# Optimization experiments

Measured on AMD Instinct MI355X. Metric: run time of the kernel, lower is better.

The kernel has to match this reference:

```python
import jax, jax.numpy as jnp
import numpy as np

EPS = 1e-5

def _ln(x, g, b):
    mu = jnp.mean(x, axis=-1, keepdims=True)
    var = jnp.mean((x - mu) ** 2, axis=-1, keepdims=True)
    return (x - mu) / jnp.sqrt(var + EPS) * g + b

def _silu(x):
    return x * jax.nn.sigmoid(x)

def setup_inputs() -> dict:
    key = jax.random.key(0)
    ks = jax.random.split(key, 32)
    B = 131072
    def rn(k, shape, scale=0.05):
        return jax.random.normal(k, shape, dtype=jnp.float32) * scale
    inp = {
        'x': jax.random.normal(ks[0], (B, 90), dtype=jnp.float32),
        'w_emb': rn(ks[1], (24, 10)),
        'pos_d': rn(ks[2], (9, 24), 0.02),
        'pos_c': rn(ks[3], (3, 64), 0.02),
        'tw1': rn(ks[4], (256, 72)), 'tb1': rn(ks[5], (256,)),
        'tw2': rn(ks[6], (256, 256)), 'tb2': rn(ks[7], (256,)),
        'tw3': rn(ks[8], (64, 256)), 'tb3': jnp.zeros((64,), jnp.float32),
        'ln1g': jnp.ones((64,), jnp.float32), 'ln1b': jnp.zeros((64,), jnp.float32),
        'inpw': rn(ks[9], (192, 64)), 'inpb': rn(ks[10], (192,)),
        'outw': rn(ks[11], (64, 64)), 'outb': rn(ks[12], (64,)),
        'ln2g': jnp.ones((64,), jnp.float32), 'ln2b': jnp.zeros((64,), jnp.float32),
        'ffw1': rn(ks[13], (128, 64)), 'ffb1': rn(ks[14], (128,)),
        'ffw2': rn(ks[15], (64, 128)), 'ffb2': rn(ks[16], (64,)),
        'hw1': rn(ks[17], (160, 192)), 'hb1': rn(ks[18], (160,)),
        'hw2': rn(ks[19], (64, 160)), 'hb2': rn(ks[20], (64,)),
        'hw3': rn(ks[21], (1, 64)), 'hb3': jnp.zeros((1,), jnp.float32),
    }
    return inp

def reference(x, w_emb, pos_d, pos_c, tw1, tb1, tw2, tb2, tw3, tb3,
              ln1g, ln1b, inpw, inpb, outw, outb, ln2g, ln2b,
              ffw1, ffb1, ffw2, ffb2, hw1, hb1, hw2, hb2, hw3, hb3):
    B = x.shape[0]
    H, D = 4, 16  # heads, head_dim (embed 64)
    digits = x.reshape(B, 9, 10) @ w_emb.T + pos_d          # [B,9,24]
    chunks = digits.reshape(B, 3, 72)                        # [B,3,72]
    h = _silu(chunks @ tw1.T + tb1)                          # [B,3,256]
    h = _silu(h @ tw2.T + tb2)                               # [B,3,256]
    chunks = h @ tw3.T + tb3                                 # [B,3,64]
    chunks = chunks + pos_c
    a = _ln(chunks, ln1g, ln1b)
    qkv = a @ inpw.T + inpb                                  # [B,3,192]
    q, k, v = jnp.split(qkv, 3, axis=-1)
    q = q.reshape(B, 3, H, D).transpose(0, 2, 1, 3)
    k = k.reshape(B, 3, H, D).transpose(0, 2, 1, 3)
    v = v.reshape(B, 3, H, D).transpose(0, 2, 1, 3)
    scores = jnp.einsum('bhsd,bhtd->bhst', q, k) / jnp.sqrt(jnp.float32(D))
    attn = jax.nn.softmax(scores, axis=-1)
    o = jnp.einsum('bhst,bhtd->bhsd', attn, v)
    o = o.transpose(0, 2, 1, 3).reshape(B, 3, 64)
    attn_out = o @ outw.T + outb
    chunks = chunks + attn_out
    f = _ln(chunks, ln2g, ln2b)
    chunks = chunks + (_silu(f @ ffw1.T + ffb1) @ ffw2.T + ffb2)
    flat = chunks.reshape(B, 192)
    hh = _silu(flat @ hw1.T + hb1)
    hh = _silu(hh @ hw2.T + hb2)
    return hh @ hw3.T + hb3                                  # [B,1]
```

## Files before the change

kernel.cpp:

```cpp
#include <hip/hip_runtime.h>
#include <math.h>


typedef short s8v __attribute__((ext_vector_type(8)));
typedef float f4v __attribute__((ext_vector_type(4)));
typedef int   i2v __attribute__((ext_vector_type(2)));
typedef int   i4v __attribute__((ext_vector_type(4)));

__device__ __forceinline__ short f2bf(float f) {
    unsigned u = __float_as_uint(f);
    unsigned r = (u + 0x7fffu + ((u >> 16) & 1u)) >> 16;
    return (short)r;
}
__device__ __forceinline__ int cvt_pk_bf16(float a, float b) {
    int r;
    asm("v_cvt_pk_bf16_f32 %0, %1, %2" : "=v"(r) : "v"(a), "v"(b));
    return r;
}
__device__ __forceinline__ float silu_f(float v) {
    return v * __builtin_amdgcn_rcpf(1.0f + __expf(-v));
}

#define BARRIER() do {                                        \
    asm volatile("s_waitcnt lgkmcnt(0)" ::: "memory");        \
    __builtin_amdgcn_s_barrier();                             \
    __builtin_amdgcn_sched_barrier(0);                        \
} while (0)

#define OFF_T1F  0
#define OFF_TW2  8192
#define OFF_TW3  73728
#define OFF_INP  90112
#define OFF_OUT  102400
#define OFF_FF1  106496
#define OFF_FF2  114688
#define OFF_HW1  122880
#define OFF_HW2  153600
#define BIAS1_ELEM 163840

__global__ void pack_weights(const float* __restrict__ w_emb, const float* __restrict__ tw1,
                             const float* __restrict__ pos_d, const float* __restrict__ tb1,
                             const float* __restrict__ tw2, const float* __restrict__ tw3,
                             const float* __restrict__ inpw, const float* __restrict__ outw,
                             const float* __restrict__ ffw1, const float* __restrict__ ffw2,
                             const float* __restrict__ hw1, const float* __restrict__ hw2,
                             short* __restrict__ dst)
{
    int L = blockIdx.y;
    if (L == 0) {
        int total = 16 * 512;
        for (int e = blockIdx.x * blockDim.x + threadIdx.x; e < total; e += gridDim.x * blockDim.x) {
            int nt = e >> 9, q = e & 511;
            int l = q >> 3, j = q & 7;
            int n = nt * 16 + (l & 15);
            int k = (l >> 4) * 8 + j;
            float v = 0.f;
            if (k < 30) {
                int gl = k / 10, kk = k - gl * 10;
                const float* trow = tw1 + n * 72 + gl * 24;
                for (int jj = 0; jj < 24; ++jj) v += trow[jj] * w_emb[jj * 10 + kk];
            }
            dst[OFF_T1F + e] = f2bf(v);
        }
        return;
    }
    if (L == 9) {
        float* b1 = (float*)(dst + BIAS1_ELEM);
        for (int e = blockIdx.x * blockDim.x + threadIdx.x; e < 768; e += gridDim.x * blockDim.x) {
            int pos = e >> 8, n = e & 255;
            float v = tb1[n];
            for (int j = 0; j < 72; ++j)
                v += tw1[n * 72 + j] * pos_d[(pos * 3 + j / 24) * 24 + (j % 24)];
            b1[e] = v;
        }
        return;
    }
    const float* W; int K, KS, N, off;
    switch (L) {
      case 1: W = tw2;  K = 256; KS = 8; N = 256; off = OFF_TW2; break;
      case 2: W = tw3;  K = 256; KS = 8; N = 64;  off = OFF_TW3; break;
      case 3: W = inpw; K = 64;  KS = 2; N = 192; off = OFF_INP; break;
      case 4: W = outw; K = 64;  KS = 2; N = 64;  off = OFF_OUT; break;
      case 5: W = ffw1; K = 64;  KS = 2; N = 128; off = OFF_FF1; break;
      case 6: W = ffw2; K = 128; KS = 4; N = 64;  off = OFF_FF2; break;
      case 7: W = hw1;  K = 192; KS = 6; N = 160; off = OFF_HW1; break;
      default:W = hw2;  K = 160; KS = 5; N = 64;  off = OFF_HW2; break;
    }
    int total = (N >> 4) * KS * 512;
    for (int e = blockIdx.x * blockDim.x + threadIdx.x; e < total; e += gridDim.x * blockDim.x) {
        int nt = e / (KS * 512);
        int r  = e - nt * (KS * 512);
        int ks = r >> 9;
        int q  = r & 511;
        int l  = q >> 3, j = q & 7;
        int n  = nt * 16 + (l & 15);
        int k  = ks * 32 + (l >> 4) * 8 + j;
        dst[off + e] = f2bf((k < K) ? W[n * K + k] : 0.0f);
    }
}

template<int KSH> struct PreW { s8v w[KSH]; };

template<int KSH>
__device__ __forceinline__ PreW<KSH> preloadW(const short* __restrict__ Wp,
                                              int lane, int nt, int ksTotal) {
    PreW<KSH> p;
    #pragma unroll
    for (int ks = 0; ks < KSH; ++ks)
        p.w[ks] = *(const s8v*)(Wp + nt * (ksTotal * 512) + ks * 512 + lane * 8);
    return p;
}

template<int EPI, int OP>
__device__ __forceinline__ void epi_store(f4v acc, f4v bv, int t, int n0, void* Out,
                                          const float* __restrict__ aux)
{
    if (EPI == 0 || EPI == 1) {
        float v0 = acc[0] + bv[0], v1 = acc[1] + bv[1];
        float v2 = acc[2] + bv[2], v3 = acc[3] + bv[3];
        if (EPI == 0) { v0 = silu_f(v0); v1 = silu_f(v1); v2 = silu_f(v2); v3 = silu_f(v3); }
        i2v pk; pk[0] = cvt_pk_bf16(v0, v1); pk[1] = cvt_pk_bf16(v2, v3);
        *(i2v*)((short*)Out + t * OP + n0) = pk;
    } else if (EPI == 2) {
        f4v* p = (f4v*)((float*)Out + t * OP + n0);
        f4v o = *p;
        #pragma unroll
        for (int i = 0; i < 4; ++i) o[i] += acc[i] + bv[i];
        *p = o;
    } else if (EPI == 3) {
        f4v pc = *(const f4v*)(aux + (t % 3) * 64 + n0);
        f4v o;
        #pragma unroll
        for (int i = 0; i < 4; ++i) o[i] = acc[i] + bv[i] + pc[i];
        *(f4v*)((float*)Out + t * OP + n0) = o;
    } else if (EPI == 5) {
        f4v ch = *(const f4v*)(aux + t * 68 + n0);
        int rr = t / 3, cc = t - rr * 3;
        i2v pk;
        pk[0] = cvt_pk_bf16(ch[0] + acc[0] + bv[0], ch[1] + acc[1] + bv[1]);
        pk[1] = cvt_pk_bf16(ch[2] + acc[2] + bv[2], ch[3] + acc[3] + bv[3]);
        *(i2v*)((short*)Out + rr * OP + cc * 64 + n0) = pk;
    } else if (EPI == 6) {
        f4v w = *(const f4v*)(aux + n0);
        float p = silu_f(acc[0] + bv[0]) * w[0] + silu_f(acc[1] + bv[1]) * w[1]
                + silu_f(acc[2] + bv[2]) * w[2] + silu_f(acc[3] + bv[3]) * w[3];
        ((float*)Out)[t * OP + (n0 >> 2)] = p;
    } else {
        f4v bp = *(const f4v*)(aux + (t % 3) * 256 + n0);
        float v0 = silu_f(acc[0] + bp[0]), v1 = silu_f(acc[1] + bp[1]);
        float v2 = silu_f(acc[2] + bp[2]), v3 = silu_f(acc[3] + bp[3]);
        i2v pk; pk[0] = cvt_pk_bf16(v0, v1); pk[1] = cvt_pk_bf16(v2, v3);
        *(i2v*)((short*)Out + t * OP + n0) = pk;
    }
}

template<int MT, int KS, int EPI, int AP, int OP>
__device__ __forceinline__ void mfma_T(
    const short* __restrict__ Wp,
    const float* __restrict__ bias,
    const short* A, void* Out, int N,
    const float* __restrict__ aux, int lane, int wid, PreW<KS> pre)
{
    const int l15 = lane & 15, l4 = lane >> 4;
    s8v xf[MT][KS];
    #pragma unroll
    for (int m = 0; m < MT; ++m)
        #pragma unroll
        for (int ks = 0; ks < KS; ++ks)
            xf[m][ks] = *(const s8v*)(A + (m * 16 + l15) * AP + ks * 32 + l4 * 8);

    s8v wf[KS];
    #pragma unroll
    for (int ks = 0; ks < KS; ++ks) wf[ks] = pre.w[ks];

    const int NT = N >> 4;
    for (int nt = wid; nt < NT; nt += 4) {
        s8v wfn[KS];
        const bool more = (nt + 4) < NT;
        if (more) {
            #pragma unroll
            for (int ks = 0; ks < KS; ++ks)
                wfn[ks] = *(const s8v*)(Wp + (nt + 4) * (KS * 512) + ks * 512 + lane * 8);
        }
        const int n0 = nt * 16 + l4 * 4;
        f4v bv = {0.f, 0.f, 0.f, 0.f};
        if (EPI != 7) bv = *(const f4v*)(bias + n0);
        #pragma unroll
        for (int m = 0; m < MT; ++m) {
            f4v acc = {0.f, 0.f, 0.f, 0.f};
            #pragma unroll
            for (int ks = 0; ks < KS; ++ks)
                acc = __builtin_amdgcn_mfma_f32_16x16x32_bf16(wf[ks], xf[m][ks], acc, 0, 0, 0);
            epi_store<EPI, OP>(acc, bv, m * 16 + l15, n0, Out, aux);
        }
        if (more) {
            #pragma unroll
            for (int ks = 0; ks < KS; ++ks) wf[ks] = wfn[ks];
        }
    }
}

template<int OP>
__device__ __forceinline__ void mfma_x1(
    const short* __restrict__ Wp, const float* __restrict__ x, long long row0,
    void* Out, const float* __restrict__ bias1,
    int lane, int wid, PreW<1> pre)
{
    const int l15 = lane & 15, l4 = lane >> 4;
    s8v xf[3];
    #pragma unroll
    for (int m = 0; m < 3; ++m) {
        int t = m * 16 + l15;
        int r = t / 3, c = t - r * 3;
        const float* xp = x + (row0 + r) * 90 + c * 30 + l4 * 8;
        float2 a = *(const float2*)xp;
        float2 b = *(const float2*)(xp + 2);
        float2 d = *(const float2*)(xp + 4);
        float2 e = (l4 < 3) ? *(const float2*)(xp + 6) : make_float2(0.f, 0.f);
        i4v pk;
        pk[0] = cvt_pk_bf16(a.x, a.y);
        pk[1] = cvt_pk_bf16(b.x, b.y);
        pk[2] = cvt_pk_bf16(d.x, d.y);
        pk[3] = cvt_pk_bf16(e.x, e.y);
        xf[m] = *(s8v*)&pk;
    }

    s8v wf = pre.w[0];
    for (int nt = wid; nt < 16; nt += 4) {
        s8v wfn;
        const bool more = (nt + 4) < 16;
        if (more) wfn = *(const s8v*)(Wp + (nt + 4) * 512 + lane * 8);
        const int n0 = nt * 16 + l4 * 4;
        #pragma unroll
        for (int m = 0; m < 3; ++m) {
            f4v acc = {0.f, 0.f, 0.f, 0.f};
            acc = __builtin_amdgcn_mfma_f32_16x16x32_bf16(wf, xf[m], acc, 0, 0, 0);
            epi_store<7, OP>(acc, acc, m * 16 + l15, n0, Out, bias1);
        }
        if (more) wf = wfn;
    }
}

template<int AP>
__device__ __forceinline__ void mfma_tw2_inplace(
    const short* __restrict__ Wp, const float* __restrict__ bias,
    short* H, int lane, int wid, PreW<2> pre)
{
    const int l15 = lane & 15, l4 = lane >> 4;
    f4v acc[4][3];
    #pragma unroll
    for (int i = 0; i < 4; ++i)
        #pragma unroll
        for (int m = 0; m < 3; ++m) acc[i][m] = (f4v){0.f, 0.f, 0.f, 0.f};

    s8v wf[2];
    wf[0] = pre.w[0]; wf[1] = pre.w[1];

    #pragma unroll
    for (int kh = 0; kh < 4; ++kh) {
        s8v xf[3][2];
        #pragma unroll
        for (int m = 0; m < 3; ++m)
            #pragma unroll
            for (int ks = 0; ks < 2; ++ks)
                xf[m][ks] = *(const s8v*)(H + (m * 16 + l15) * AP + (kh * 2 + ks) * 32 + l4 * 8);
        #pragma unroll
        for (int i = 0; i < 4; ++i) {
            s8v wfn[2];
            const bool more = (i < 3) || (kh < 3);
            if (more) {
                const int ni  = (i < 3) ? i + 1 : 0;
                const int nkh = (i < 3) ? kh : kh + 1;
                const int nnt = wid + ni * 4;
                #pragma unroll
                for (int ks = 0; ks < 2; ++ks)
                    wfn[ks] = *(const s8v*)(Wp + nnt * (8 * 512) + (nkh * 2 + ks) * 512 + lane * 8);
            }
            #pragma unroll
            for (int m = 0; m < 3; ++m) {
                acc[i][m] = __builtin_amdgcn_mfma_f32_16x16x32_bf16(wf[0], xf[m][0], acc[i][m], 0, 0, 0);
                acc[i][m] = __builtin_amdgcn_mfma_f32_16x16x32_bf16(wf[1], xf[m][1], acc[i][m], 0, 0, 0);
            }
            if (more) { wf[0] = wfn[0]; wf[1] = wfn[1]; }
        }
    }

    BARRIER();

    #pragma unroll
    for (int i = 0; i < 4; ++i) {
        const int nt = wid + i * 4;
        const int n0 = nt * 16 + l4 * 4;
        f4v bv = *(const f4v*)(bias + n0);
        #pragma unroll
        for (int m = 0; m < 3; ++m)
            epi_store<0, AP>(acc[i][m], bv, m * 16 + l15, n0, H, nullptr);
    }
}

template<int MT, int KSH, int KH, int NTW, int EPI, int AP, int OP>
__device__ __forceinline__ void mfma_acc(
    const short* __restrict__ Wp, const float* __restrict__ bias,
    const short* A, void* Out,
    const float* __restrict__ aux, int lane, int wid, int ntBase, PreW<KSH> pre)
{
    const int l15 = lane & 15, l4 = lane >> 4;
    const int KS = KSH * KH;
    f4v acc[NTW][MT];
    #pragma unroll
    for (int i = 0; i < NTW; ++i)
        #pragma unroll
        for (int m = 0; m < MT; ++m) acc[i][m] = (f4v){0.f, 0.f, 0.f, 0.f};

    s8v wf[KSH];
    #pragma unroll
    for (int ks = 0; ks < KSH; ++ks) wf[ks] = pre.w[ks];

    #pragma unroll
    for (int kh = 0; kh < KH; ++kh) {
        s8v xf[MT][KSH];
        #pragma unroll
        for (int m = 0; m < MT; ++m)
            #pragma unroll
            for (int ks = 0; ks < KSH; ++ks)
                xf[m][ks] = *(const s8v*)(A + (m * 16 + l15) * AP + (kh * KSH + ks) * 32 + l4 * 8);
        #pragma unroll
        for (int i = 0; i < NTW; ++i) {
            s8v wfn[KSH];
            const bool more = (i + 1 < NTW) || (kh + 1 < KH);
            if (more) {
                const int ni  = (i + 1 < NTW) ? i + 1 : 0;
                const int nkh = (i + 1 < NTW) ? kh : kh + 1;
                const int nnt = wid + (ntBase + ni) * 4;
                #pragma unroll
                for (int ks = 0; ks < KSH; ++ks)
                    wfn[ks] = *(const s8v*)(Wp + nnt * (KS * 512) + (nkh * KSH + ks) * 512 + lane * 8);
            }
            #pragma unroll
            for (int m = 0; m < MT; ++m)
                #pragma unroll
                for (int ks = 0; ks < KSH; ++ks)
                    acc[i][m] = __builtin_amdgcn_mfma_f32_16x16x32_bf16(wf[ks], xf[m][ks], acc[i][m], 0, 0, 0);
            if (more) {
                #pragma unroll
                for (int ks = 0; ks < KSH; ++ks) wf[ks] = wfn[ks];
            }
        }
    }
    #pragma unroll
    for (int i = 0; i < NTW; ++i) {
        const int nt = wid + (ntBase + i) * 4;
        const int n0 = nt * 16 + l4 * 4;
        f4v bv = *(const f4v*)(bias + n0);
        #pragma unroll
        for (int m = 0; m < MT; ++m)
            epi_store<EPI, OP>(acc[i][m], bv, m * 16 + l15, n0, Out, aux);
    }
}

__device__ __forceinline__ void ln_phase(const float* CH, short* dst, const int dp,
                                         const float* __restrict__ g,
                                         const float* __restrict__ b, int tid)
{
    if (tid < 192) {
        int t = tid >> 2, p = tid & 3;
        const float* cp = CH + t * 68 + p * 16;
        f4v c[4];
        #pragma unroll
        for (int i = 0; i < 4; ++i) c[i] = *(const f4v*)(cp + i * 4);
        float s = 0.f, ss = 0.f;
        #pragma unroll
        for (int i = 0; i < 4; ++i)
            #pragma unroll
            for (int j = 0; j < 4; ++j) { float v = c[i][j]; s += v; ss += v * v; }
        s += __shfl_xor(s, 1); ss += __shfl_xor(ss, 1);
        s += __shfl_xor(s, 2); ss += __shfl_xor(ss, 2);
        float mu = s * (1.0f / 64.0f);
        float var = ss * (1.0f / 64.0f) - mu * mu;
        float rstd = rsqrtf(var + 1e-5f);
        int pk[8];
        #pragma unroll
        for (int i = 0; i < 4; ++i) {
            f4v gv = *(const f4v*)(g + p * 16 + i * 4);
            f4v bvv = *(const f4v*)(b + p * 16 + i * 4);
            float o0 = (c[i][0] - mu) * rstd * gv[0] + bvv[0];
            float o1 = (c[i][1] - mu) * rstd * gv[1] + bvv[1];
            float o2 = (c[i][2] - mu) * rstd * gv[2] + bvv[2];
            float o3 = (c[i][3] - mu) * rstd * gv[3] + bvv[3];
            pk[i * 2]     = cvt_pk_bf16(o0, o1);
            pk[i * 2 + 1] = cvt_pk_bf16(o2, o3);
        }
        i4v w0 = {pk[0], pk[1], pk[2], pk[3]};
        i4v w1 = {pk[4], pk[5], pk[6], pk[7]};
        *(i4v*)(dst + t * dp + p * 16) = w0;
        *(i4v*)(dst + t * dp + p * 16 + 8) = w1;
    }
}

#define LDS_BYTES 39168

__global__ __launch_bounds__(256, 4)
void towers_mfma(const float* __restrict__ x,
                 const float* __restrict__ pos_c,
                 const float* __restrict__ tb2, const float* __restrict__ tb3,
                 const float* __restrict__ ln1g, const float* __restrict__ ln1b,
                 const float* __restrict__ inpb, const float* __restrict__ outb,
                 const float* __restrict__ ln2g, const float* __restrict__ ln2b,
                 const float* __restrict__ ffb1, const float* __restrict__ ffb2,
                 const float* __restrict__ hb1, const float* __restrict__ hb2,
                 const float* __restrict__ hw3, const float* __restrict__ hb3,
                 const short* __restrict__ wsBp,
                 float* __restrict__ out)
{
    __shared__ __align__(16) char smem[LDS_BYTES];

    const int tid = threadIdx.x;
    const int lane = tid & 63, wid = tid >> 6;
    const long long row0 = (long long)blockIdx.x * 16;
    const float* bias1 = (const float*)(wsBp + BIAS1_ELEM);

    short* H    = (short*)smem;
    float* CH   = (float*)(smem + 26112);
    short* tmp7 = (short*)(smem + 19200);

    PreW<1> preT1f = preloadW<1>(wsBp + OFF_T1F, lane, wid, 1);
    mfma_x1<264>(wsBp + OFF_T1F, x, row0, H, bias1, lane, wid, preT1f);
    PreW<2> preT2 = preloadW<2>(wsBp + OFF_TW2, lane, wid, 8);
    BARRIER();

    mfma_tw2_inplace<264>(wsBp + OFF_TW2, tb2, H, lane, wid, preT2);
    PreW<4> preT3 = preloadW<4>(wsBp + OFF_TW3, lane, wid, 8);
    BARRIER();

    mfma_acc<3, 4, 2, 1, 3, 264, 68>(wsBp + OFF_TW3, tb3, H, CH, pos_c, lane, wid, 0, preT3);
    PreW<2> preINP = preloadW<2>(wsBp + OFF_INP, lane, wid, 2);
    BARRIER();

    ln_phase(CH, tmp7, 72, ln1g, ln1b, tid);
    BARRIER();

    short* qkv = (short*)smem;
    mfma_T<3, 2, 1, 72, 200>(wsBp + OFF_INP, inpb, tmp7, qkv, 192, nullptr, lane, wid, preINP);
    PreW<2> preOUT = preloadW<2>(wsBp + OFF_OUT, lane, wid, 2);
    BARRIER();

    if (tid < 192) {
        int r = tid & 15, hc = tid >> 4;
        int h = hc & 3, cq = hc >> 2;
        const short* qp = qkv + (r * 3 + cq) * 200 + h * 16;
        float qv[16];
        { s8v q0 = *(const s8v*)qp, q1 = *(const s8v*)(qp + 8);
          #pragma unroll
          for (int j = 0; j < 8; ++j) {
              qv[j] = __uint_as_float(((unsigned)(unsigned short)q0[j]) << 16);
              qv[8 + j] = __uint_as_float(((unsigned)(unsigned short)q1[j]) << 16);
          } }
        float sc[3];
        #pragma unroll
        for (int c = 0; c < 3; ++c) {
            const short* kp = qkv + (r * 3 + c) * 200 + 64 + h * 16;
            s8v k0 = *(const s8v*)kp, k1 = *(const s8v*)(kp + 8);
            float acc = 0.f;
            #pragma unroll
            for (int j = 0; j < 8; ++j) {
                acc += qv[j] * __uint_as_float(((unsigned)(unsigned short)k0[j]) << 16)
                     + qv[8 + j] * __uint_as_float(((unsigned)(unsigned short)k1[j]) << 16);
            }
            sc[c] = acc * 0.25f;
        }
        float m = fmaxf(sc[0], fmaxf(sc[1], sc[2]));
        float e0 = __expf(sc[0] - m), e1 = __expf(sc[1] - m), e2 = __expf(sc[2] - m);
        float inv = 1.0f / (e0 + e1 + e2);
        e0 *= inv; e1 *= inv; e2 *= inv;
        float ov[16];
        #pragma unroll
        for (int j = 0; j < 16; ++j) ov[j] = 0.f;
        const float ee[3] = {e0, e1, e2};
        #pragma unroll
        for (int c = 0; c < 3; ++c) {
            const short* vp = qkv + (r * 3 + c) * 200 + 128 + h * 16;
            s8v v0 = *(const s8v*)vp, v1 = *(const s8v*)(vp + 8);
            #pragma unroll
            for (int j = 0; j < 8; ++j) {
                ov[j]     += ee[c] * __uint_as_float(((unsigned)(unsigned short)v0[j]) << 16);
                ov[8 + j] += ee[c] * __uint_as_float(((unsigned)(unsigned short)v1[j]) << 16);
            }
        }
        short* op = tmp7 + (r * 3 + cq) * 72 + h * 16;
        i4v pk;
        pk[0] = cvt_pk_bf16(ov[0], ov[1]);   pk[1] = cvt_pk_bf16(ov[2], ov[3]);
        pk[2] = cvt_pk_bf16(ov[4], ov[5]);   pk[3] = cvt_pk_bf16(ov[6], ov[7]);
        *(i4v*)op = pk;
        pk[0] = cvt_pk_bf16(ov[8], ov[9]);   pk[1] = cvt_pk_bf16(ov[10], ov[11]);
        pk[2] = cvt_pk_bf16(ov[12], ov[13]); pk[3] = cvt_pk_bf16(ov[14], ov[15]);
        *(i4v*)(op + 8) = pk;
    }
    BARRIER();

    mfma_T<3, 2, 2, 72, 68>(wsBp + OFF_OUT, outb, tmp7, CH, 64, nullptr, lane, wid, preOUT);
    PreW<2> preFF1 = preloadW<2>(wsBp + OFF_FF1, lane, wid, 2);
    BARRIER();

    ln_phase(CH, tmp7, 72, ln2g, ln2b, tid);
    BARRIER();

    short* g1 = (short*)smem;
    mfma_T<3, 2, 0, 72, 136>(wsBp + OFF_FF1, ffb1, tmp7, g1, 128, nullptr, lane, wid, preFF1);
    PreW<4> preFF2 = preloadW<4>(wsBp + OFF_FF2, lane, wid, 4);
    BARRIER();
    short* flat = (short*)(smem + 13056);
    mfma_T<3, 4, 5, 136, 200>(wsBp + OFF_FF2, ffb2, g1, flat, 64, CH, lane, wid, preFF2);
    PreW<6> preH1 = preloadW<6>(wsBp + OFF_HW1, lane, wid, 6);
    BARRIER();

    short* hh1 = (short*)smem;
    mfma_T<1, 6, 0, 200, 168>(wsBp + OFF_HW1, hb1, flat, hh1, 160, nullptr, lane, wid, preH1);
    PreW<5> preH2 = preloadW<5>(wsBp + OFF_HW2, lane, wid, 5);
    BARRIER();
    float* part = (float*)(smem + 8192);
    mfma_T<1, 5, 6, 168, 16>(wsBp + OFF_HW2, hb2, hh1, part, 64, hw3, lane, wid, preH2);
    BARRIER();

    if (tid < 64) {
        int r = tid >> 2, p = tid & 3;
        const float* pp = part + r * 16 + p * 4;
        float acc = pp[0] + pp[1] + pp[2] + pp[3];
        acc += __shfl_xor(acc, 1);
        acc += __shfl_xor(acc, 2);
        if (p == 0) out[row0 + r] = acc + hb3[0];
    }
}

extern "C" void kernel_launch(void* const* d_in, const int* in_sizes, int n_in,
                              void* d_out, int out_size, void* d_ws, size_t ws_size,
                              hipStream_t stream) {
    const float* x     = (const float*)d_in[0];
    const float* w_emb = (const float*)d_in[1];
    const float* pos_d = (const float*)d_in[2];
    const float* pos_c = (const float*)d_in[3];
    const float* tw1   = (const float*)d_in[4];
    const float* tb1   = (const float*)d_in[5];
    const float* tw2   = (const float*)d_in[6];
    const float* tb2   = (const float*)d_in[7];
    const float* tw3   = (const float*)d_in[8];
    const float* tb3   = (const float*)d_in[9];
    const float* ln1g  = (const float*)d_in[10];
    const float* ln1b  = (const float*)d_in[11];
    const float* inpw  = (const float*)d_in[12];
    const float* inpb  = (const float*)d_in[13];
    const float* outw  = (const float*)d_in[14];
    const float* outb  = (const float*)d_in[15];
    const float* ln2g  = (const float*)d_in[16];
    const float* ln2b  = (const float*)d_in[17];
    const float* ffw1  = (const float*)d_in[18];
    const float* ffb1  = (const float*)d_in[19];
    const float* ffw2  = (const float*)d_in[20];
    const float* ffb2  = (const float*)d_in[21];
    const float* hw1   = (const float*)d_in[22];
    const float* hb1   = (const float*)d_in[23];
    const float* hw2   = (const float*)d_in[24];
    const float* hb2   = (const float*)d_in[25];
    const float* hw3   = (const float*)d_in[26];
    const float* hb3   = (const float*)d_in[27];
    float* out = (float*)d_out;
    short* wsBp = (short*)d_ws;

    pack_weights<<<dim3(16, 10), 256, 0, stream>>>(w_emb, tw1, pos_d, tb1,
                                                   tw2, tw3, inpw, outw,
                                                   ffw1, ffw2, hw1, hw2, wsBp);

    const int B = in_sizes[0] / 90;
    towers_mfma<<<B / 16, 256, 0, stream>>>(
        x, pos_c, tb2, tb3,
        ln1g, ln1b, inpb, outb, ln2g, ln2b,
        ffb1, ffb2, hb1, hb2, hw3, hb3, wsBp, out);
}
```

Measured before the change: 209.4 us.

## Store residual chunks in bf16 LDS and compact buffers to raise occupancy

Changes the residual stream buffer from fp32 to bf16 in shared memory, unpacking to float on reads for layer norm and residual adds. It also reassigns the scratch buffer offsets so total LDS per block shrinks, allowing launch bounds of 5 blocks per CU instead of 4. The aim is more resident waves to hide latency between the many barrier-separated phases. In exchange, residual accumulation loses precision because it is rounded to bf16 after each stage.

```diff
diff --git a/kernel.cpp b/kernel.cpp
--- a/kernel.cpp
+++ b/kernel.cpp
@@ -17,6 +17,8 @@
     asm("v_cvt_pk_bf16_f32 %0, %1, %2" : "=v"(r) : "v"(a), "v"(b));
     return r;
 }
+__device__ __forceinline__ float bf_lo(int w) { return __uint_as_float((unsigned)w << 16); }
+__device__ __forceinline__ float bf_hi(int w) { return __uint_as_float((unsigned)w & 0xffff0000u); }
 __device__ __forceinline__ float silu_f(float v) {
     return v * __builtin_amdgcn_rcpf(1.0f + __expf(-v));
 }
@@ -113,7 +115,7 @@
 
 template<int EPI, int OP>
 __device__ __forceinline__ void epi_store(f4v acc, f4v bv, int t, int n0, void* Out,
-                                          const float* __restrict__ aux)
+                                          const void* aux)
 {
     if (EPI == 0 || EPI == 1) {
         float v0 = acc[0] + bv[0], v1 = acc[1] + bv[1];
@@ -122,31 +124,35 @@
         i2v pk; pk[0] = cvt_pk_bf16(v0, v1); pk[1] = cvt_pk_bf16(v2, v3);
         *(i2v*)((short*)Out + t * OP + n0) = pk;
     } else if (EPI == 2) {
-        f4v* p = (f4v*)((float*)Out + t * OP + n0);
-        f4v o = *p;
-        #pragma unroll
-        for (int i = 0; i < 4; ++i) o[i] += acc[i] + bv[i];
-        *p = o;
+        i2v* p = (i2v*)((short*)Out + t * 68 + n0);
+        i2v c = *p;
+        float o0 = bf_lo(c[0]) + acc[0] + bv[0];
+        float o1 = bf_hi(c[0]) + acc[1] + bv[1];
+        float o2 = bf_lo(c[1]) + acc[2] + bv[2];
+        float o3 = bf_hi(c[1]) + acc[3] + bv[3];
+        i2v pk; pk[0] = cvt_pk_bf16(o0, o1); pk[1] = cvt_pk_bf16(o2, o3);
+        *p = pk;
     } else if (EPI == 3) {
-        f4v pc = *(const f4v*)(aux + (t % 3) * 64 + n0);
-        f4v o;
-        #pragma unroll
-        for (int i = 0; i < 4; ++i) o[i] = acc[i] + bv[i] + pc[i];
-        *(f4v*)((float*)Out + t * OP + n0) = o;
+        const float* pc = (const float*)aux + (t % 3) * 64 + n0;
+        i2v pk;
+        pk[0] = cvt_pk_bf16(acc[0] + bv[0] + pc[0], acc[1] + bv[1] + pc[1]);
+        pk[1] = cvt_pk_bf16(acc[2] + bv[2] + pc[2], acc[3] + bv[3] + pc[3]);
+        *(i2v*)((short*)Out + t * 68 + n0) = pk;
     } else if (EPI == 5) {
-        f4v ch = *(const f4v*)(aux + t * 68 + n0);
+        const short* chb = (const short*)aux;
+        i2v c = *(const i2v*)(chb + t * 68 + n0);
         int rr = t / 3, cc = t - rr * 3;
         i2v pk;
-        pk[0] = cvt_pk_bf16(ch[0] + acc[0] + bv[0], ch[1] + acc[1] + bv[1]);
-        pk[1] = cvt_pk_bf16(ch[2] + acc[2] + bv[2], ch[3] + acc[3] + bv[3]);
+        pk[0] = cvt_pk_bf16(bf_lo(c[0]) + acc[0] + bv[0], bf_hi(c[0]) + acc[1] + bv[1]);
+        pk[1] = cvt_pk_bf16(bf_lo(c[1]) + acc[2] + bv[2], bf_hi(c[1]) + acc[3] + bv[3]);
         *(i2v*)((short*)Out + rr * OP + cc * 64 + n0) = pk;
     } else if (EPI == 6) {
-        f4v w = *(const f4v*)(aux + n0);
+        const float* w = (const float*)aux + n0;
         float p = silu_f(acc[0] + bv[0]) * w[0] + silu_f(acc[1] + bv[1]) * w[1]
                 + silu_f(acc[2] + bv[2]) * w[2] + silu_f(acc[3] + bv[3]) * w[3];
         ((float*)Out)[t * OP + (n0 >> 2)] = p;
     } else {
-        f4v bp = *(const f4v*)(aux + (t % 3) * 256 + n0);
+        const float* bp = (const float*)aux + (t % 3) * 256 + n0;
         float v0 = silu_f(acc[0] + bp[0]), v1 = silu_f(acc[1] + bp[1]);
         float v2 = silu_f(acc[2] + bp[2]), v3 = silu_f(acc[3] + bp[3]);
         i2v pk; pk[0] = cvt_pk_bf16(v0, v1); pk[1] = cvt_pk_bf16(v2, v3);
@@ -159,7 +165,7 @@
     const short* __restrict__ Wp,
     const float* __restrict__ bias,
     const short* A, void* Out, int N,
-    const float* __restrict__ aux, int lane, int wid, PreW<KS> pre)
+    const void* aux, int lane, int wid, PreW<KS> pre)
 {
     const int l15 = lane & 15, l4 = lane >> 4;
     s8v xf[MT][KS];
@@ -302,7 +308,7 @@
 __device__ __forceinline__ void mfma_acc(
     const short* __restrict__ Wp, const float* __restrict__ bias,
     const short* A, void* Out,
-    const float* __restrict__ aux, int lane, int wid, int ntBase, PreW<KSH> pre)
+    const void* aux, int lane, int wid, int ntBase, PreW<KSH> pre)
 {
     const int l15 = lane & 15, l4 = lane >> 4;
     const int KS = KSH * KH;
@@ -358,21 +364,23 @@
     }
 }
 
-__device__ __forceinline__ void ln_phase(const float* CH, short* dst, const int dp,
+__device__ __forceinline__ void ln_phase(const short* CHb, short* dst, const int dp,
                                          const float* __restrict__ g,
                                          const float* __restrict__ b, int tid)
 {
     if (tid < 192) {
         int t = tid >> 2, p = tid & 3;
-        const float* cp = CH + t * 68 + p * 16;
-        f4v c[4];
-        #pragma unroll
-        for (int i = 0; i < 4; ++i) c[i] = *(const f4v*)(cp + i * 4);
+        const short* cp = CHb + t * 68 + p * 16;
+        float c[16];
+        #pragma unroll
+        for (int i = 0; i < 4; ++i) {
+            i2v w = *(const i2v*)(cp + i * 4);
+            c[i * 4 + 0] = bf_lo(w[0]); c[i * 4 + 1] = bf_hi(w[0]);
+            c[i * 4 + 2] = bf_lo(w[1]); c[i * 4 + 3] = bf_hi(w[1]);
+        }
         float s = 0.f, ss = 0.f;
         #pragma unroll
-        for (int i = 0; i < 4; ++i)
-            #pragma unroll
-            for (int j = 0; j < 4; ++j) { float v = c[i][j]; s += v; ss += v * v; }
+        for (int i = 0; i < 16; ++i) { s += c[i]; ss += c[i] * c[i]; }
         s += __shfl_xor(s, 1); ss += __shfl_xor(ss, 1);
         s += __shfl_xor(s, 2); ss += __shfl_xor(ss, 2);
         float mu = s * (1.0f / 64.0f);
@@ -383,10 +391,10 @@
         for (int i = 0; i < 4; ++i) {
             f4v gv = *(const f4v*)(g + p * 16 + i * 4);
             f4v bvv = *(const f4v*)(b + p * 16 + i * 4);
-            float o0 = (c[i][0] - mu) * rstd * gv[0] + bvv[0];
-            float o1 = (c[i][1] - mu) * rstd * gv[1] + bvv[1];
-            float o2 = (c[i][2] - mu) * rstd * gv[2] + bvv[2];
-            float o3 = (c[i][3] - mu) * rstd * gv[3] + bvv[3];
+            float o0 = (c[i * 4 + 0] - mu) * rstd * gv[0] + bvv[0];
+            float o1 = (c[i * 4 + 1] - mu) * rstd * gv[1] + bvv[1];
+            float o2 = (c[i * 4 + 2] - mu) * rstd * gv[2] + bvv[2];
+            float o3 = (c[i * 4 + 3] - mu) * rstd * gv[3] + bvv[3];
             pk[i * 2]     = cvt_pk_bf16(o0, o1);
             pk[i * 2 + 1] = cvt_pk_bf16(o2, o3);
         }
@@ -397,9 +405,9 @@
     }
 }
 
-#define LDS_BYTES 39168
-
-__global__ __launch_bounds__(256, 4)
+#define LDS_BYTES 32640
+
+__global__ __launch_bounds__(256, 5)
 void towers_mfma(const float* __restrict__ x,
                  const float* __restrict__ pos_c,
                  const float* __restrict__ tb2, const float* __restrict__ tb3,
@@ -420,8 +428,9 @@
     const float* bias1 = (const float*)(wsBp + BIAS1_ELEM);
 
     short* H    = (short*)smem;
-    float* CH   = (float*)(smem + 26112);
-    short* tmp7 = (short*)(smem + 19200);
+    short* CHb  = (short*)(smem + 26112);
+    short* tmp7 = (short*)smem;
+    short* qkv  = (short*)(smem + 6912);
 
     PreW<1> preT1f = preloadW<1>(wsBp + OFF_T1F, lane, wid, 1);
     mfma_x1<264>(wsBp + OFF_T1F, x, row0, H, bias1, lane, wid, preT1f);
@@ -432,14 +441,13 @@
     PreW<4> preT3 = preloadW<4>(wsBp + OFF_TW3, lane, wid, 8);
     BARRIER();
 
-    mfma_acc<3, 4, 2, 1, 3, 264, 68>(wsBp + OFF_TW3, tb3, H, CH, pos_c, lane, wid, 0, preT3);
+    mfma_acc<3, 4, 2, 1, 3, 264, 68>(wsBp + OFF_TW3, tb3, H, CHb, pos_c, lane, wid, 0, preT3);
     PreW<2> preINP = preloadW<2>(wsBp + OFF_INP, lane, wid, 2);
     BARRIER();
 
-    ln_phase(CH, tmp7, 72, ln1g, ln1b, tid);
-    BARRIER();
-
-    short* qkv = (short*)smem;
+    ln_phase(CHb, tmp7, 72, ln1g, ln1b, tid);
+    BARRIER();
+
     mfma_T<3, 2, 1, 72, 200>(wsBp + OFF_INP, inpb, tmp7, qkv, 192, nullptr, lane, wid, preINP);
     PreW<2> preOUT = preloadW<2>(wsBp + OFF_OUT, lane, wid, 2);
     BARRIER();
@@ -497,27 +505,27 @@
     }
     BARRIER();
 
-    mfma_T<3, 2, 2, 72, 68>(wsBp + OFF_OUT, outb, tmp7, CH, 64, nullptr, lane, wid, preOUT);
+    mfma_T<3, 2, 2, 72, 68>(wsBp + OFF_OUT, outb, tmp7, CHb, 64, nullptr, lane, wid, preOUT);
     PreW<2> preFF1 = preloadW<2>(wsBp + OFF_FF1, lane, wid, 2);
     BARRIER();
 
-    ln_phase(CH, tmp7, 72, ln2g, ln2b, tid);
-    BARRIER();
-
-    short* g1 = (short*)smem;
+    ln_phase(CHb, tmp7, 72, ln2g, ln2b, tid);
+    BARRIER();
+
+    short* g1 = (short*)(smem + 6912);
     mfma_T<3, 2, 0, 72, 136>(wsBp + OFF_FF1, ffb1, tmp7, g1, 128, nullptr, lane, wid, preFF1);
     PreW<4> preFF2 = preloadW<4>(wsBp + OFF_FF2, lane, wid, 4);
     BARRIER();
-    short* flat = (short*)(smem + 13056);
-    mfma_T<3, 4, 5, 136, 200>(wsBp + OFF_FF2, ffb2, g1, flat, 64, CH, lane, wid, preFF2);
+    short* flat = (short*)smem;
+    mfma_T<3, 4, 5, 136, 200>(wsBp + OFF_FF2, ffb2, g1, flat, 64, CHb, lane, wid, preFF2);
     PreW<6> preH1 = preloadW<6>(wsBp + OFF_HW1, lane, wid, 6);
     BARRIER();
 
-    short* hh1 = (short*)smem;
+    short* hh1 = (short*)(smem + 6912);
     mfma_T<1, 6, 0, 200, 168>(wsBp + OFF_HW1, hb1, flat, hh1, 160, nullptr, lane, wid, preH1);
     PreW<5> preH2 = preloadW<5>(wsBp + OFF_HW2, lane, wid, 5);
     BARRIER();
-    float* part = (float*)(smem + 8192);
+    float* part = (float*)smem;
     mfma_T<1, 5, 6, 168, 16>(wsBp + OFF_HW2, hb2, hh1, part, 64, hw3, lane, wid, preH2);
     BARRIER();
 
```

Measured after the change: 279.6 us. +33.5%, slower.
